# Performance work log

Hardware: AMD Instinct MI355X
Metric: run time of the kernel (lower is better)

The kernel has to match this reference:

```python
import jax, jax.numpy as jnp
import numpy as np

B, NP, NR = 4, 2048, 10
EDGE_F = 32
EMB = 64          # emb_features == out_features (required for layer stacking)
ESM_EMB = 64
HEADS = 16
NUM_LAYERS = 4
LN_EPS = 1e-5


def _ln(x, g, b):
    mu = jnp.mean(x, axis=-1, keepdims=True)
    var = jnp.var(x, axis=-1, keepdims=True)
    return (x - mu) / jnp.sqrt(var + LN_EPS) * g + b


def setup_inputs() -> dict:
    key = jax.random.key(0)
    ks = jax.random.split(key, 32)
    s = 0.05  # xavier-ish scale for weights
    inp = {
        "pep_feat": jax.random.normal(ks[0], (B, NP, 27 + 1280), jnp.float32),
        "rec_feat": jax.random.normal(ks[1], (B, NP, NR, 42 + 1280), jnp.float32),
        "edge_feat": jax.random.normal(ks[2], (B, NP, NR, EDGE_F), jnp.float32),
        # embedding weights (torch Linear convention: y = x @ W.T)
        "W_rec_esm": jax.random.normal(ks[3], (ESM_EMB, 1280), jnp.float32) * s,
        "W_pep_esm": jax.random.normal(ks[4], (ESM_EMB, 1280), jnp.float32) * s,
        "W_pep_emb": jax.random.normal(ks[5], (EMB, 27 + ESM_EMB), jnp.float32) * s,
        "W_rec_emb": jax.random.normal(ks[6], (EMB, 21 + ESM_EMB), jnp.float32) * s,
        "W_edge_emb": jax.random.normal(ks[7], (EMB, EDGE_F), jnp.float32) * s,
        "pep_ln_g": jnp.ones((EMB,), jnp.float32),
        "pep_ln_b": jnp.zeros((EMB,), jnp.float32),
        "rec_ln_g": jnp.ones((EMB,), jnp.float32),
        "rec_ln_b": jnp.zeros((EMB,), jnp.float32),
        # stacked GraphAttention layer params [L, ...]
        "ga_Wp": jax.random.normal(ks[8], (NUM_LAYERS, EMB, EMB), jnp.float32) * s,
        "ga_bp": jnp.zeros((NUM_LAYERS, EMB), jnp.float32),
        "ga_Wr": jax.random.normal(ks[9], (NUM_LAYERS, EMB, 2 * EMB), jnp.float32) * s,
        "ga_br": jnp.zeros((NUM_LAYERS, EMB), jnp.float32),
        "ga_Wv": jax.random.normal(ks[10], (NUM_LAYERS, EMB, 2 * EMB), jnp.float32) * s,
        "ga_bv": jnp.zeros((NUM_LAYERS, EMB), jnp.float32),
        # self-attention pooling: LN + MLP [64 -> 64 -> 32 -> 16 heads], no biases
        "pool_ln_g": jnp.ones((EMB,), jnp.float32),
        "pool_ln_b": jnp.zeros((EMB,), jnp.float32),
        "pool_W0": jax.random.normal(ks[11], (EMB, EMB), jnp.float32) * s,
        "pool_W1": jax.random.normal(ks[12], (EMB // 2, EMB), jnp.float32) * s,
        "pool_W2": jax.random.normal(ks[13], (HEADS, EMB // 2), jnp.float32) * s,
        # final projection
        "mlp_W": jax.random.normal(ks[14], (EMB // 2, EMB), jnp.float32) * s,
        "mlp_b": jnp.zeros((EMB // 2,), jnp.float32),
    }
    return inp


def _forward(pep_feat, rec_feat, edge_feat, W_rec_esm, W_pep_esm, W_pep_emb,
             W_rec_emb, W_edge_emb, pep_ln_g, pep_ln_b, rec_ln_g, rec_ln_b,
             ga_Wp, ga_bp, ga_Wr, ga_br, ga_Wv, ga_bv,
             pool_ln_g, pool_ln_b, pool_W0, pool_W1, pool_W2, mlp_W, mlp_b):
    # --- embeddings ---
    rec_esm = rec_feat[..., 42:] @ W_rec_esm.T                       # [B,NP,10,ESM]
    pep_esm = pep_feat[..., -1280:] @ W_pep_esm.T                    # [B,NP,ESM]
    rec = jnp.concatenate([rec_feat[..., :21], rec_esm], axis=-1) @ W_rec_emb.T
    pep = jnp.concatenate([pep_feat[..., :27], pep_esm], axis=-1) @ W_pep_emb.T
    edge = edge_feat @ W_edge_emb.T                                  # [B,NP,10,EMB]
    pep = _ln(pep, pep_ln_g, pep_ln_b)
    rec = _ln(rec, rec_ln_g, rec_ln_b)

    inv_sqrt_d = 1.0 / np.sqrt(EMB).astype(np.float32)
    rec_edge = jnp.concatenate([rec, edge], axis=-1)                 # [B,NP,10,2*EMB]
    # --- stacked GraphAttention layers (dropout = eval-mode identity) ---
    for l in range(NUM_LAYERS):
        q = pep @ ga_Wp[l].T + ga_bp[l]                              # [B,NP,EMB]
        key = rec_edge @ ga_Wr[l].T + ga_br[l]                       # [B,NP,10,EMB]
        val = rec_edge @ ga_Wv[l].T + ga_bv[l]                       # [B,NP,10,EMB]
        logit = jnp.einsum('bpd,bprd->bpr', q, key) * inv_sqrt_d     # [B,NP,10]
        attn = jax.nn.softmax(logit, axis=-1)
        pep = q + jnp.einsum('bpr,bprd->bpd', attn, val)             # [B,NP,EMB]

    # --- self-attention pooling (note: softmax applied twice, as in source) ---
    d = _ln(pep, pool_ln_g, pool_ln_b)                               # [B,NP,EMB]
    h = jnp.tanh(d @ pool_W0.T)
    h = jnp.tanh(h @ pool_W1.T)
    logits = h @ pool_W2.T                                           # [B,NP,HEADS]
    a = jax.nn.softmax(logits, axis=1)
    a = jax.nn.softmax(a, axis=1)
    attended = jnp.einsum('bsh,bsd->bhd', a, d)                      # [B,HEADS,EMB]
    pooled = attended.mean(axis=1)                                   # [B,EMB]
    return pooled @ mlp_W.T + mlp_b                                  # [B,EMB//2]


def reference(pep_feat, rec_feat, edge_feat, W_rec_esm, W_pep_esm, W_pep_emb,
              W_rec_emb, W_edge_emb, pep_ln_g, pep_ln_b, rec_ln_g, rec_ln_b,
              ga_Wp, ga_bp, ga_Wr, ga_br, ga_Wv, ga_bv,
              pool_ln_g, pool_ln_b, pool_W0, pool_W1, pool_W2, mlp_W, mlp_b):
    return _forward(pep_feat, rec_feat, edge_feat, W_rec_esm, W_pep_esm, W_pep_emb,
                    W_rec_emb, W_edge_emb, pep_ln_g, pep_ln_b, rec_ln_g, rec_ln_b,
                    ga_Wp, ga_bp, ga_Wr, ga_br, ga_Wv, ga_bv,
                    pool_ln_g, pool_ln_b, pool_W0, pool_W1, pool_W2, mlp_W, mlp_b)
```

## Files before the change

kernel.cpp:

```cpp
#include <hip/hip_runtime.h>
#include <hip/hip_bf16.h>


typedef __attribute__((ext_vector_type(8))) short bf16x8;
typedef __attribute__((ext_vector_type(4))) float f32x4;

#define MFMA(a, b, c) __builtin_amdgcn_mfma_f32_16x16x32_bf16((a), (b), (c), 0, 0, 0)

#define WB_REC_OFF   0
#define WB_PEP_OFF   83968
#define WB_EDGE_OFF  167936
#define WB_P_OFF     169984
#define WB_R_OFF     186368
#define WB_V_OFF     219136
#define WB_W0_OFF    251904
#define WB_W1_OFF    256000
#define WB_W2_OFF    258048
#define WB_TOTAL     258560

__device__ __forceinline__ unsigned short f2bf(float x) {
  __hip_bfloat16 h = __float2bfloat16(x);
  return __builtin_bit_cast(unsigned short, h);
}
__device__ __forceinline__ float bf2f(unsigned short u) {
  unsigned int t = ((unsigned int)u) << 16;
  return __builtin_bit_cast(float, t);
}
__device__ __forceinline__ bf16x8 loadBc(const unsigned short* base, int chunk, int lane) {
  return *(const bf16x8*)(base + ((size_t)chunk * 64 + lane) * 8);
}
__device__ __forceinline__ float tanhf_fast(float x) {
  float e = __expf(2.f * x);
  return 1.f - 2.f / (e + 1.f);
}

__global__ __launch_bounds__(256) void k_pack(
    const float* __restrict__ Wresm, const float* __restrict__ Wpesm,
    const float* __restrict__ Wre, const float* __restrict__ Wpe,
    const float* __restrict__ Wedge, const float* __restrict__ Wp,
    const float* __restrict__ Wr, const float* __restrict__ Wv,
    const float* __restrict__ W0, const float* __restrict__ W1,
    const float* __restrict__ W2, unsigned short* __restrict__ WB) {
  const int t = blockIdx.x * 256 + threadIdx.x;
  if (t >= WB_TOTAL) return;
  float v = 0.f;
  if (t < WB_EDGE_OFF) {
    bool isPep = (t >= WB_PEP_OFF);
    int u = isPep ? (t - WB_PEP_OFF) : t;
    int j = u & 7, lane = (u >> 3) & 63, n = (u >> 9) & 3, kc = u >> 11;
    int k = kc * 32 + ((lane >> 4) << 3) + j;
    int col = n * 16 + (lane & 15);
    if (kc < 40) {
      const float* wemb = isPep ? (Wpe + col * 91 + 27) : (Wre + col * 85 + 21);
      const float* wesm = isPep ? Wpesm : Wresm;
      float s = 0.f;
#pragma unroll 8
      for (int e = 0; e < 64; ++e) s += wemb[e] * wesm[e * 1280 + k];
      v = s;
    } else {
      int kl = k - 1280;
      if (isPep) v = (kl < 27) ? Wpe[col * 91 + kl] : 0.f;
      else       v = (kl < 21) ? Wre[col * 85 + kl] : 0.f;
    }
  } else if (t < WB_P_OFF) {
    int u = t - WB_EDGE_OFF;
    int j = u & 7, lane = (u >> 3) & 63, n = (u >> 9) & 3;
    v = Wedge[(n * 16 + (lane & 15)) * 32 + ((lane >> 4) << 3) + j];
  } else if (t < WB_R_OFF) {
    int u = t - WB_P_OFF;
    int l = u >> 12, w = u & 4095;
    int j = w & 7, lane = (w >> 3) & 63, n = (w >> 9) & 3, kc = w >> 11;
    int o = kc * 32 + ((lane >> 4) << 3) + j;
    int d = n * 16 + (lane & 15);
    v = Wp[l * 4096 + d * 64 + o];
  } else if (t < WB_V_OFF) {
    int u = t - WB_R_OFF;
    int l = u >> 13, w = u & 8191;
    int j = w & 7, lane = (w >> 3) & 63, c = (w >> 9) & 15;
    int kc = c >> 3, n = c & 7;
    int o = kc * 32 + ((lane >> 4) << 3) + j;
    int k = n * 16 + (lane & 15);
    v = Wr[l * 8192 + o * 128 + k];
  } else if (t < WB_W0_OFF) {
    int u = t - WB_V_OFF;
    int l = u >> 13, w = u & 8191;
    int j = w & 7, lane = (w >> 3) & 63, n = (w >> 9) & 3, kc = w >> 11;
    int k = kc * 32 + ((lane >> 4) << 3) + j;
    int d = n * 16 + (lane & 15);
    v = Wv[l * 8192 + d * 128 + k];
  } else if (t < WB_W1_OFF) {
    int u = t - WB_W0_OFF;
    int j = u & 7, lane = (u >> 3) & 63, c = u >> 9;
    int kc = c >> 2, n = c & 3;
    v = W0[(n * 16 + (lane & 15)) * 64 + kc * 32 + ((lane >> 4) << 3) + j];
  } else if (t < WB_W2_OFF) {
    int u = t - WB_W1_OFF;
    int j = u & 7, lane = (u >> 3) & 63, c = u >> 9;
    int kc = c >> 1, n = c & 1;
    v = W1[(n * 16 + (lane & 15)) * 64 + kc * 32 + ((lane >> 4) << 3) + j];
  } else {
    int u = t - WB_W2_OFF;
    int j = u & 7, lane = (u >> 3) & 63;
    v = W2[(lane & 15) * 32 + ((lane >> 4) << 3) + j];
  }
  WB[t] = f2bf(v);
}

__global__ __launch_bounds__(64) void k_emb(
    const float* __restrict__ rec_feat, const float* __restrict__ edge_feat,
    const float* __restrict__ pep_feat, const unsigned short* __restrict__ WB,
    const float* __restrict__ rec_g, const float* __restrict__ rec_b,
    const float* __restrict__ pep_g, const float* __restrict__ pep_b,
    unsigned short* __restrict__ rec_edge, unsigned short* __restrict__ pep_out) {
  __shared__ unsigned short stg[2][16][128];
  const int bid = blockIdx.x;
  const int lane = threadIdx.x;
  const int quad = lane >> 4, lr = lane & 15;
  const bool isPep = (bid >= 5120);
  const int brow = (isPep ? bid - 5120 : bid) * 16;
  const float* __restrict__ src = isPep ? pep_feat : rec_feat;
  const int rowlen = isPep ? 1307 : 1322;
  const int head = isPep ? 27 : 42;
  const unsigned short* WBb = WB + (isPep ? WB_PEP_OFF : WB_REC_OFF);

  const f32x4 fz = {0.f, 0.f, 0.f, 0.f};
  f32x4 acc[4] = {fz, fz, fz, fz};

  float lx[16], ly[16];

  auto loadg = [&](int g) {
    if (!isPep) {
#pragma unroll
      for (int i = 0; i < 16; ++i) {
        const float2 v =
            *(const float2*)(src + (size_t)(brow + i) * 1322 + 42 + g * 128 + lane * 2);
        lx[i] = v.x; ly[i] = v.y;
      }
    } else {
#pragma unroll
      for (int i = 0; i < 16; ++i) {
        const float* p = src + (size_t)(brow + i) * 1307 + 27 + g * 128 + lane * 2;
        lx[i] = p[0]; ly[i] = p[1];
      }
    }
  };
  auto writeg = [&](int b) {
#pragma unroll
    for (int i = 0; i < 16; ++i) {
      const unsigned u = (unsigned)f2bf(lx[i]) | ((unsigned)f2bf(ly[i]) << 16);
      *(unsigned*)((char*)&stg[b][i][0] +
                   ((((lane >> 2) ^ i) << 4) | ((lane & 3) << 2))) = u;
    }
  };
  auto frag = [&](int b, int kc) -> bf16x8 {
    return *(const bf16x8*)((const char*)&stg[b][lr][0] +
                            ((((kc << 2) | quad) ^ lr) << 4));
  };

  loadg(0); writeg(0);
  int buf = 0;
  for (int g = 0; g < 10; ++g) {
    bf16x8 bb[16];
#pragma unroll
    for (int m = 0; m < 16; ++m) bb[m] = loadBc(WBb, g * 16 + m, lane);
    if (g < 9) loadg(g + 1);
#pragma unroll
    for (int c = 0; c < 4; ++c) {
      const bf16x8 a = frag(buf, c);
#pragma unroll
      for (int n = 0; n < 4; ++n) acc[n] = MFMA(a, bb[c * 4 + n], acc[n]);
    }
    if (g < 9) writeg(buf ^ 1);
    buf ^= 1;
  }
  {
    const float* p = src + (size_t)(brow + lr) * rowlen + quad * 8;
    bf16x8 a;
    if (!isPep) {
#pragma unroll
      for (int m = 0; m < 4; ++m) {
        const float2 v = *(const float2*)(p + 2 * m);
        a[2 * m] = (short)f2bf(v.x); a[2 * m + 1] = (short)f2bf(v.y);
      }
    } else {
#pragma unroll
      for (int j = 0; j < 8; ++j) a[j] = (short)f2bf(p[j]);
    }
#pragma unroll
    for (int n = 0; n < 4; ++n)
      acc[n] = MFMA(a, loadBc(WBb, 160 + n, lane), acc[n]);
  }

  float s[4], sq[4];
#pragma unroll
  for (int i = 0; i < 4; ++i) {
    s[i] = acc[0][i] + acc[1][i] + acc[2][i] + acc[3][i];
    sq[i] = acc[0][i] * acc[0][i] + acc[1][i] * acc[1][i] +
            acc[2][i] * acc[2][i] + acc[3][i] * acc[3][i];
  }
#pragma unroll
  for (int msk = 1; msk < 16; msk <<= 1) {
#pragma unroll
    for (int i = 0; i < 4; ++i) {
      s[i] += __shfl_xor(s[i], msk);
      sq[i] += __shfl_xor(sq[i], msk);
    }
  }
  const float* gp = isPep ? pep_g : rec_g;
  const float* bp = isPep ? pep_b : rec_b;
  float gv[4], bvl[4];
#pragma unroll
  for (int n = 0; n < 4; ++n) { gv[n] = gp[lr + 16 * n]; bvl[n] = bp[lr + 16 * n]; }

  if (!isPep) {
    f32x4 acce[4] = {fz, fz, fz, fz};
    {
      const float* p = edge_feat + (size_t)(brow + lr) * 32 + quad * 8;
      const float4 f0 = *(const float4*)(p);
      const float4 f1 = *(const float4*)(p + 4);
      bf16x8 a;
#pragma unroll
      for (int j = 0; j < 4; ++j) { a[j] = (short)f2bf(f0[j]); a[4 + j] = (short)f2bf(f1[j]); }
#pragma unroll
      for (int n = 0; n < 4; ++n) acce[n] = MFMA(a, loadBc(WB + WB_EDGE_OFF, n, lane), acce[n]);
    }
#pragma unroll
    for (int i = 0; i < 4; ++i) {
      const float mean = s[i] * (1.f / 64.f);
      const float var = sq[i] * (1.f / 64.f) - mean * mean;
      const float rstd = rsqrtf(var + 1e-5f);
      unsigned short* dst = rec_edge + (size_t)(brow + quad * 4 + i) * 128;
#pragma unroll
      for (int n = 0; n < 4; ++n) {
        dst[lr + 16 * n] = f2bf((acc[n][i] - mean) * rstd * gv[n] + bvl[n]);
        dst[64 + lr + 16 * n] = f2bf(acce[n][i]);
      }
    }
  } else {
#pragma unroll
    for (int i = 0; i < 4; ++i) {
      const float mean = s[i] * (1.f / 64.f);
      const float var = sq[i] * (1.f / 64.f) - mean * mean;
      const float rstd = rsqrtf(var + 1e-5f);
      unsigned short* dst = pep_out + (size_t)(brow + quad * 4 + i) * 64;
#pragma unroll
      for (int n = 0; n < 4; ++n)
        dst[lr + 16 * n] = f2bf((acc[n][i] - mean) * rstd * gv[n] + bvl[n]);
    }
  }
}

__global__ __launch_bounds__(256) void k_ga(
    const unsigned short* __restrict__ rec_edge, const unsigned short* __restrict__ pep_bf,
    const unsigned short* __restrict__ WB,
    const float* __restrict__ ga_bp, const float* __restrict__ ga_bv,
    const float* __restrict__ pool_g, const float* __restrict__ pool_b,
    float* __restrict__ dbuf, float* __restrict__ logitsT) {
  __shared__ unsigned short pep_s[1024];
  __shared__ unsigned short q_s[1024];
  __shared__ __align__(16) unsigned short zs[2048];
  __shared__ float bias_s[512];
  __shared__ float lgp[4][10][17];
  __shared__ float redp[4][2][16];
  __shared__ float oap[4][16][68];

  const int tid = threadIdx.x;
  const int w = tid >> 6;
  const int lane = tid & 63;
  const int quad = lane >> 4, lr = lane & 15;
  const int swz = lr & 7;
  const int pbase = blockIdx.x * 16;
  const int mycol = lr + 16 * w;
  const f32x4 fz = {0.f, 0.f, 0.f, 0.f};

  bias_s[tid] = ga_bp[tid & 255];
  bias_s[256 + tid] = ga_bv[tid & 255];
  if (tid < 128) {
    const int p = tid >> 3, gg = tid & 7;
    const bf16x8 v = *(const bf16x8*)(pep_bf + (size_t)(pbase + p) * 64 + gg * 8);
    *(bf16x8*)(pep_s + p * 64 + ((gg ^ (p & 7)) << 3)) = v;
  }
  const unsigned short* reb =
      rec_edge + (size_t)(pbase + lr) * 1280 + w * 32 + quad * 8;
  bf16x8 rfs[10];
#pragma unroll
  for (int r = 0; r < 10; ++r) rfs[r] = *(const bf16x8*)(reb + r * 128);
  __syncthreads();

  auto bwrite = [&](unsigned short* buf, int p, int col, unsigned short val) {
    buf[p * 64 + ((((col >> 3)) ^ (p & 7)) << 3) + (col & 7)] = val;
  };
  auto bfrag = [&](const unsigned short* buf, int kc) -> bf16x8 {
    return *(const bf16x8*)(buf + lr * 64 + ((((kc << 2) + quad) ^ swz) << 3));
  };

  f32x4 pcur;
  for (int l = 0; l < 4; ++l) {
    const unsigned short* WBp = WB + WB_P_OFF + l * 4096;
    const unsigned short* WBr = WB + WB_R_OFF + l * 8192;
    const unsigned short* WBv = WB + WB_V_OFF + l * 8192;

    f32x4 qa = fz;
    qa = MFMA(bfrag(pep_s, 0), loadBc(WBp, w, lane), qa);
    qa = MFMA(bfrag(pep_s, 1), loadBc(WBp, 4 + w, lane), qa);
    const float bpv = bias_s[l * 64 + mycol];
#pragma unroll
    for (int i = 0; i < 4; ++i) qa[i] += bpv;
#pragma unroll
    for (int i = 0; i < 4; ++i) bwrite(q_s, quad * 4 + i, mycol, f2bf(qa[i]));
    __syncthreads();

    const bf16x8 aq0 = bfrag(q_s, 0), aq1 = bfrag(q_s, 1);
    f32x4 za0 = fz, za1 = fz;
    za0 = MFMA(aq0, loadBc(WBr, 2 * w, lane), za0);
    za0 = MFMA(aq1, loadBc(WBr, 8 + 2 * w, lane), za0);
    za1 = MFMA(aq0, loadBc(WBr, 2 * w + 1, lane), za1);
    za1 = MFMA(aq1, loadBc(WBr, 9 + 2 * w, lane), za1);
#pragma unroll
    for (int i = 0; i < 4; ++i) {
      const int p = quad * 4 + i;
      const int k0 = 16 * (2 * w) + lr, k1 = 16 * (2 * w + 1) + lr;
      zs[p * 128 + ((((k0 >> 3) ^ (p & 7)) << 3) | (k0 & 7))] = f2bf(za0[i]);
      zs[p * 128 + ((((k1 >> 3) ^ (p & 7)) << 3) | (k1 & 7))] = f2bf(za1[i]);
    }
    float zfw[8];
    {
      const bf16x8 z8 = *(const bf16x8*)(zs + lr * 128 + (((quad + 4 * w) ^ swz) << 3));
#pragma unroll
      for (int j = 0; j < 8; ++j) zfw[j] = bf2f((unsigned short)z8[j]);
    }
#pragma unroll
    for (int r = 0; r < 10; ++r) {
      float part = 0.f;
#pragma unroll
      for (int j = 0; j < 8; ++j) part += bf2f((unsigned short)rfs[r][j]) * zfw[j];
      part += __shfl_xor(part, 16);
      part += __shfl_xor(part, 32);
      if (quad == 0) lgp[w][r][lr] = part;
    }
    __syncthreads();
    float lg[10];
#pragma unroll
    for (int r = 0; r < 10; ++r)
      lg[r] = (lgp[0][r][lr] + lgp[1][r][lr] + lgp[2][r][lr] + lgp[3][r][lr]) * 0.125f;
    float mx = lg[0];
#pragma unroll
    for (int r = 1; r < 10; ++r) mx = fmaxf(mx, lg[r]);
    float ssum = 0.f;
#pragma unroll
    for (int r = 0; r < 10; ++r) { lg[r] = __expf(lg[r] - mx); ssum += lg[r]; }
    const float inv = 1.f / ssum;
#pragma unroll
    for (int r = 0; r < 10; ++r) lg[r] *= inv;
    float wsacc[8] = {};
#pragma unroll
    for (int r = 0; r < 10; ++r)
#pragma unroll
      for (int j = 0; j < 8; ++j)
        wsacc[j] += lg[r] * bf2f((unsigned short)rfs[r][j]);
    bf16x8 wf;
#pragma unroll
    for (int j = 0; j < 8; ++j) wf[j] = (short)f2bf(wsacc[j]);
    f32x4 oa[4];
#pragma unroll
    for (int n = 0; n < 4; ++n) oa[n] = MFMA(wf, loadBc(WBv, w * 4 + n, lane), fz);
#pragma unroll
    for (int n = 0; n < 4; ++n)
#pragma unroll
      for (int i = 0; i < 4; ++i)
        oap[w][quad * 4 + i][n * 16 + lr] = oa[n][i];
    __syncthreads();
    const float bvv = bias_s[256 + l * 64 + mycol];
#pragma unroll
    for (int i = 0; i < 4; ++i) {
      const int p = quad * 4 + i;
      const float o = oap[0][p][mycol] + oap[1][p][mycol] +
                      oap[2][p][mycol] + oap[3][p][mycol];
      pcur[i] = qa[i] + o + bvv;
    }
#pragma unroll
    for (int i = 0; i < 4; ++i) bwrite(pep_s, quad * 4 + i, mycol, f2bf(pcur[i]));
    __syncthreads();
  }

  {
    float s[4], sq[4];
#pragma unroll
    for (int i = 0; i < 4; ++i) { s[i] = pcur[i]; sq[i] = pcur[i] * pcur[i]; }
#pragma unroll
    for (int msk = 1; msk < 16; msk <<= 1) {
#pragma unroll
      for (int i = 0; i < 4; ++i) {
        s[i] += __shfl_xor(s[i], msk);
        sq[i] += __shfl_xor(sq[i], msk);
      }
    }
    if (lr == 0) {
#pragma unroll
      for (int i = 0; i < 4; ++i) {
        redp[w][0][quad * 4 + i] = s[i];
        redp[w][1][quad * 4 + i] = sq[i];
      }
    }
    __syncthreads();
    const float gv = pool_g[mycol], bv2 = pool_b[mycol];
    float d[4];
    float* zf32 = (float*)zs;
#pragma unroll
    for (int i = 0; i < 4; ++i) {
      const int p = quad * 4 + i;
      const float sf = redp[0][0][p] + redp[1][0][p] + redp[2][0][p] + redp[3][0][p];
      const float sqf = redp[0][1][p] + redp[1][1][p] + redp[2][1][p] + redp[3][1][p];
      const float mean = sf * (1.f / 64.f);
      const float var = sqf * (1.f / 64.f) - mean * mean;
      const float rstd = rsqrtf(var + 1e-5f);
      d[i] = (pcur[i] - mean) * rstd * gv + bv2;
      zf32[p * 64 + mycol] = d[i];
      bwrite(q_s, p, mycol, f2bf(d[i]));
    }
    __syncthreads();
    {
      const float4 v = *(const float4*)(&zf32[tid * 4]);
      *(float4*)(dbuf + (size_t)pbase * 64 + tid * 4) = v;
    }
    if (w == 0) {
      const bf16x8 ad0 = bfrag(q_s, 0), ad1 = bfrag(q_s, 1);
      f32x4 h0[4] = {fz, fz, fz, fz};
#pragma unroll
      for (int n = 0; n < 4; ++n) {
        h0[n] = MFMA(ad0, loadBc(WB + WB_W0_OFF, n, lane), h0[n]);
        h0[n] = MFMA(ad1, loadBc(WB + WB_W0_OFF, 4 + n, lane), h0[n]);
      }
#pragma unroll
      for (int n = 0; n < 4; ++n)
#pragma unroll
        for (int i = 0; i < 4; ++i)
          bwrite(q_s, quad * 4 + i, lr + 16 * n, f2bf(tanhf_fast(h0[n][i])));
      const bf16x8 ah00 = bfrag(q_s, 0), ah01 = bfrag(q_s, 1);
      f32x4 h1[2] = {fz, fz};
#pragma unroll
      for (int n = 0; n < 2; ++n) {
        h1[n] = MFMA(ah00, loadBc(WB + WB_W1_OFF, n, lane), h1[n]);
        h1[n] = MFMA(ah01, loadBc(WB + WB_W1_OFF, 2 + n, lane), h1[n]);
      }
#pragma unroll
      for (int n = 0; n < 2; ++n)
#pragma unroll
        for (int i = 0; i < 4; ++i)
          bwrite(q_s, quad * 4 + i, lr + 16 * n, f2bf(tanhf_fast(h1[n][i])));
      const bf16x8 ah1 = bfrag(q_s, 0);
      f32x4 lac = MFMA(ah1, loadBc(WB + WB_W2_OFF, 0, lane), fz);
      const int b = pbase >> 11, sx0 = pbase & 2047;
#pragma unroll
      for (int i = 0; i < 4; ++i)
        logitsT[(size_t)(b * 16 + lr) * 2048 + sx0 + quad * 4 + i] = lac[i];
    }
  }
}

__global__ __launch_bounds__(256) void k_pool2(
    const float* __restrict__ logitsT, const float* __restrict__ dbuf,
    float* __restrict__ attp) {
  __shared__ float sh[2048];
  __shared__ float red[8];
  __shared__ float part[16][64];
  const int blk = blockIdx.x;
  const int bh = blk >> 2, q = blk & 3;
  const int b = bh >> 4;
  const int tid = threadIdx.x, lane = tid & 63, wid = tid >> 6;
  const float* lrow = logitsT + (size_t)bh * 2048;

  float m = -1e30f;
  for (int sx = tid; sx < 2048; sx += 256) {
    float v = lrow[sx];
    sh[sx] = v;
    m = fmaxf(m, v);
  }
#pragma unroll
  for (int msk = 1; msk < 64; msk <<= 1) m = fmaxf(m, __shfl_xor(m, msk));
  if (lane == 0) red[wid] = m;
  __syncthreads();
  m = fmaxf(fmaxf(red[0], red[1]), fmaxf(red[2], red[3]));

  float s1 = 0.f;
  for (int sx = tid; sx < 2048; sx += 256) {
    float e = __expf(sh[sx] - m);
    sh[sx] = e;
    s1 += e;
  }
#pragma unroll
  for (int msk = 1; msk < 64; msk <<= 1) s1 += __shfl_xor(s1, msk);
  __syncthreads();
  if (lane == 0) red[4 + wid] = s1;
  __syncthreads();
  s1 = red[4] + red[5] + red[6] + red[7];
  const float invS1 = 1.f / s1;

  float s2 = 0.f;
  for (int sx = tid; sx < 2048; sx += 256) {
    float e2 = __expf((sh[sx] - 1.f) * invS1);
    sh[sx] = e2;
    s2 += e2;
  }
#pragma unroll
  for (int msk = 1; msk < 64; msk <<= 1) s2 += __shfl_xor(s2, msk);
  __syncthreads();
  if (lane == 0) red[wid] = s2;
  __syncthreads();
  s2 = red[0] + red[1] + red[2] + red[3];
  const float invS2 = 1.f / s2;

  const int d16 = tid & 15, sxg = tid >> 4;
  float4 a4 = {0.f, 0.f, 0.f, 0.f};
  const float* db = dbuf + (size_t)b * 2048 * 64 + d16 * 4;
#pragma unroll 4
  for (int sx = q * 512 + sxg; sx < (q + 1) * 512; sx += 16) {
    const float w = sh[sx];
    const float4 v = *(const float4*)(db + (size_t)sx * 64);
    a4.x += w * v.x; a4.y += w * v.y; a4.z += w * v.z; a4.w += w * v.w;
  }
  *(float4*)(&part[sxg][d16 * 4]) = a4;
  __syncthreads();
  if (tid < 64) {
    float s = 0.f;
#pragma unroll
    for (int g2 = 0; g2 < 16; ++g2) s += part[g2][tid];
    attp[(size_t)(bh * 4 + q) * 64 + tid] = s * invS2;
  }
}

__global__ __launch_bounds__(256) void k_final(
    const float* __restrict__ attp, const float* __restrict__ W,
    const float* __restrict__ bias, float* __restrict__ out) {
  __shared__ float pooled[4][64];
  const int tid = threadIdx.x;
  {
    const int b = tid >> 6, d = tid & 63;
    float s = 0.f;
#pragma unroll
    for (int hq = 0; hq < 64; ++hq) s += attp[((size_t)b * 64 + hq) * 64 + d];
    pooled[b][d] = s * (1.f / 16.f);
  }
  __syncthreads();
  if (tid < 128) {
    const int b = tid >> 5, j = tid & 31;
    float s = bias[j];
#pragma unroll
    for (int d2 = 0; d2 < 64; ++d2) s += pooled[b][d2] * W[j * 64 + d2];
    out[b * 32 + j] = s;
  }
}

extern "C" void kernel_launch(void* const* d_in, const int* in_sizes, int n_in,
                              void* d_out, int out_size, void* d_ws, size_t ws_size,
                              hipStream_t stream) {
  const float* pep_feat = (const float*)d_in[0];
  const float* rec_feat = (const float*)d_in[1];
  const float* edge_feat = (const float*)d_in[2];
  const float* W_rec_esm = (const float*)d_in[3];
  const float* W_pep_esm = (const float*)d_in[4];
  const float* W_pep_emb = (const float*)d_in[5];
  const float* W_rec_emb = (const float*)d_in[6];
  const float* W_edge_emb = (const float*)d_in[7];
  const float* pep_ln_g = (const float*)d_in[8];
  const float* pep_ln_b = (const float*)d_in[9];
  const float* rec_ln_g = (const float*)d_in[10];
  const float* rec_ln_b = (const float*)d_in[11];
  const float* ga_Wp = (const float*)d_in[12];
  const float* ga_bp = (const float*)d_in[13];
  const float* ga_Wr = (const float*)d_in[14];
  const float* ga_br = (const float*)d_in[15];
  const float* ga_Wv = (const float*)d_in[16];
  const float* ga_bv = (const float*)d_in[17];
  const float* pool_ln_g = (const float*)d_in[18];
  const float* pool_ln_b = (const float*)d_in[19];
  const float* pool_W0 = (const float*)d_in[20];
  const float* pool_W1 = (const float*)d_in[21];
  const float* pool_W2 = (const float*)d_in[22];
  const float* mlp_W = (const float*)d_in[23];
  const float* mlp_b = (const float*)d_in[24];
  float* out = (float*)d_out;
  (void)ga_br;
  (void)ws_size; (void)in_sizes; (void)n_in; (void)out_size;

  char* ws = (char*)d_ws;
  unsigned short* WB = (unsigned short*)(ws);
  unsigned short* rec_edge = (unsigned short*)(ws + 524288);
  unsigned short* pep_bf = (unsigned short*)(ws + 21495808);
  float* dbuf = (float*)(ws + 22544384);
  float* logitsT = (float*)(ws + 24641536);
  float* attp = (float*)(ws + 25165824);

  k_pack<<<1010, 256, 0, stream>>>(W_rec_esm, W_pep_esm, W_rec_emb, W_pep_emb,
                                   W_edge_emb, ga_Wp, ga_Wr, ga_Wv,
                                   pool_W0, pool_W1, pool_W2, WB);
  k_emb<<<5632, 64, 0, stream>>>(rec_feat, edge_feat, pep_feat, WB,
                                 rec_ln_g, rec_ln_b, pep_ln_g, pep_ln_b,
                                 rec_edge, pep_bf);
  k_ga<<<512, 256, 0, stream>>>(rec_edge, pep_bf, WB, ga_bp, ga_bv,
                                pool_ln_g, pool_ln_b, dbuf, logitsT);
  k_pool2<<<256, 256, 0, stream>>>(logitsT, dbuf, attp);
  k_final<<<1, 256, 0, stream>>>(attp, mlp_W, mlp_b, out);
}
```

Before: 176.4 us.

## Deepen embedding-kernel prefetch to two stages with fp32 triple-buffered LDS staging

```diff
diff --git a/kernel.cpp b/kernel.cpp
--- a/kernel.cpp
+++ b/kernel.cpp
@@ -32,6 +32,9 @@
 __device__ __forceinline__ float tanhf_fast(float x) {
   float e = __expf(2.f * x);
   return 1.f - 2.f / (e + 1.f);
+}
+__device__ __forceinline__ int swzr(int r) {
+  return (r & 1) | (((r >> 1) & 7) << 2);
 }
 
 __global__ __launch_bounds__(256) void k_pack(
@@ -112,7 +115,7 @@
     const float* __restrict__ rec_g, const float* __restrict__ rec_b,
     const float* __restrict__ pep_g, const float* __restrict__ pep_b,
     unsigned short* __restrict__ rec_edge, unsigned short* __restrict__ pep_out) {
-  __shared__ unsigned short stg[2][16][128];
+  __shared__ float stg[3][16][128];
   const int bid = blockIdx.x;
   const int lane = threadIdx.x;
   const int quad = lane >> 4, lr = lane & 15;
@@ -126,52 +129,59 @@
   const f32x4 fz = {0.f, 0.f, 0.f, 0.f};
   f32x4 acc[4] = {fz, fz, fz, fz};
 
-  float lx[16], ly[16];
-
-  auto loadg = [&](int g) {
+  float lx[2][16], ly[2][16];
+
+  auto loadg = [&](int s, int g) {
     if (!isPep) {
 #pragma unroll
       for (int i = 0; i < 16; ++i) {
         const float2 v =
             *(const float2*)(src + (size_t)(brow + i) * 1322 + 42 + g * 128 + lane * 2);
-        lx[i] = v.x; ly[i] = v.y;
+        lx[s][i] = v.x; ly[s][i] = v.y;
       }
     } else {
 #pragma unroll
       for (int i = 0; i < 16; ++i) {
         const float* p = src + (size_t)(brow + i) * 1307 + 27 + g * 128 + lane * 2;
-        lx[i] = p[0]; ly[i] = p[1];
+        lx[s][i] = p[0]; ly[s][i] = p[1];
       }
     }
   };
-  auto writeg = [&](int b) {
+  auto writeg = [&](int b, int s) {
 #pragma unroll
     for (int i = 0; i < 16; ++i) {
-      const unsigned u = (unsigned)f2bf(lx[i]) | ((unsigned)f2bf(ly[i]) << 16);
-      *(unsigned*)((char*)&stg[b][i][0] +
-                   ((((lane >> 2) ^ i) << 4) | ((lane & 3) << 2))) = u;
+      const int su = (lane >> 1) ^ swzr(i);
+      float2 v; v.x = lx[s][i]; v.y = ly[s][i];
+      *(float2*)((char*)&stg[b][i][0] + su * 16 + (lane & 1) * 8) = v;
     }
   };
-  auto frag = [&](int b, int kc) -> bf16x8 {
-    return *(const bf16x8*)((const char*)&stg[b][lr][0] +
-                            ((((kc << 2) | quad) ^ lr) << 4));
+  auto frag = [&](int b, int c) -> bf16x8 {
+    const int u0 = c * 8 + quad * 2;
+    const int s0 = u0 ^ swzr(lr), s1 = (u0 + 1) ^ swzr(lr);
+    const float4 f0 = *(const float4*)((const char*)&stg[b][lr][0] + s0 * 16);
+    const float4 f1 = *(const float4*)((const char*)&stg[b][lr][0] + s1 * 16);
+    bf16x8 a;
+#pragma unroll
+    for (int j = 0; j < 4; ++j) { a[j] = (short)f2bf(f0[j]); a[4 + j] = (short)f2bf(f1[j]); }
+    return a;
   };
 
-  loadg(0); writeg(0);
-  int buf = 0;
+  loadg(0, 0);
+  loadg(1, 1);
+  writeg(0, 0);
+#pragma unroll
   for (int g = 0; g < 10; ++g) {
+    if (g < 8) loadg(g & 1, g + 2);
     bf16x8 bb[16];
 #pragma unroll
     for (int m = 0; m < 16; ++m) bb[m] = loadBc(WBb, g * 16 + m, lane);
-    if (g < 9) loadg(g + 1);
 #pragma unroll
     for (int c = 0; c < 4; ++c) {
-      const bf16x8 a = frag(buf, c);
+      const bf16x8 a = frag(g % 3, c);
 #pragma unroll
       for (int n = 0; n < 4; ++n) acc[n] = MFMA(a, bb[c * 4 + n], acc[n]);
     }
-    if (g < 9) writeg(buf ^ 1);
-    buf ^= 1;
+    if (g < 9) writeg((g + 1) % 3, (g + 1) & 1);
   }
   {
     const float* p = src + (size_t)(brow + lr) * rowlen + quad * 8;
```

Measured after the change: 176.8 us. Within noise of the previous version (+0.2%).
